# Kernel tuning notes

Hardware: AMD Instinct MI355X
Metric: run time of the kernel (lower is better)

Reference implementation:

```python
import jax, jax.numpy as jnp
import numpy as np

N, D, H, B, K = 65536, 64, 128, 16, 16
EPS = 0.0

def setup_inputs() -> dict:
    key = jax.random.key(0)
    ks = jax.random.split(key, 5)
    x = jax.random.normal(ks[0], (N, D), dtype=jnp.float32)
    pos = jax.random.normal(ks[1], (N, 3), dtype=jnp.float32)
    batch = (jnp.arange(N, dtype=jnp.int32) // (N // B)).astype(jnp.int32)
    W1 = jax.random.normal(ks[2], (D, H), dtype=jnp.float32) * (1.0 / np.sqrt(D))
    b1 = jnp.zeros((H,), dtype=jnp.float32)
    W2 = jax.random.normal(ks[3], (H, D), dtype=jnp.float32) * (1.0 / np.sqrt(H))
    b2 = jnp.zeros((D,), dtype=jnp.float32)
    return {"x": x, "pos": pos, "batch": batch, "W1": W1, "b1": b1, "W2": W2, "b2": b2}

def reference(x, pos, batch, W1, b1, W2, b2):
    # batch is assumed contiguous with B equal segments of n nodes each
    n = N // B
    pos_s = pos.reshape(B, n, 3)
    x_s = x.reshape(B, n, D)
    # pairwise squared distances per segment via gram trick: [B, n, n]
    sq = jnp.sum(pos_s * pos_s, axis=-1)
    d2 = sq[:, :, None] + sq[:, None, :] - 2.0 * jnp.einsum('bic,bjc->bij', pos_s, pos_s)
    # exclude self-loops (loop=False in knn_graph)
    d2 = jnp.where(jnp.eye(n, dtype=bool)[None], jnp.inf, d2)
    # k nearest neighbors per node: indices [B, n, K]
    _, idx = jax.lax.top_k(-d2, K)
    # GIN sum aggregation: gather neighbor features and sum over K
    nb = x_s[jnp.arange(B)[:, None, None], idx]        # [B, n, K, D]
    agg = nb.sum(axis=2).reshape(N, D)                  # [N, D]
    h = (1.0 + EPS) * x + agg
    h = jax.nn.relu(h @ W1 + b1)
    out = h @ W2 + b2
    return out
```

## Files before the change

kernel.cpp:

```cpp
#include <hip/hip_runtime.h>
#include <math.h>

#define DIM  64
#define HID  128
#define KNN  16
#define SEG  1024
#define TSZ  128
#define CAP  12

typedef unsigned long long u64;
#define INF_BITS 0x7F800000u

__device__ __forceinline__ void ins16(float (&bd)[KNN], int (&bi)[KNN],
                                      float d, int g) {
    float cd = d; int ci = g;
    #pragma unroll
    for (int i = 0; i < KNN; ++i) {
        bool lt = cd < bd[i];
        float dl = lt ? cd : bd[i];
        float dh = lt ? bd[i] : cd;
        int   il = lt ? ci : bi[i];
        int   ih = lt ? bi[i] : ci;
        bd[i] = dl; bi[i] = il; cd = dh; ci = ih;
    }
}

__device__ __forceinline__ void drain_buf(const u64* bufe, int tid,
        float (&bd)[KNN], int (&bi)[KNN], int& cnt,
        unsigned* thrU, int l) {
    for (int t = 0; t < CAP; ++t) {
        if (__ballot(t < cnt) == 0ull) break;
        u64 e = bufe[t * 256 + tid];
        float d = __uint_as_float((unsigned)e);
        int   g = (int)(e >> 32);
        if ((t < cnt) && (d < bd[KNN - 1])) ins16(bd, bi, d, g);
    }
    cnt = 0;
    atomicMin(&thrU[l], __float_as_uint(bd[KNN - 1]));
}

struct f2 { float a, b; };
__device__ __forceinline__ f2 f2mul(f2 x, float s) {
    #pragma clang fp contract(off)
    f2 r; r.a = x.a * s; r.b = x.b * s; return r;
}
__device__ __forceinline__ f2 f2add(f2 x, f2 y) {
    #pragma clang fp contract(off)
    f2 r; r.a = x.a + y.a; r.b = x.b + y.b; return r;
}
__device__ __forceinline__ f2 f2adds(f2 x, float s) {
    #pragma clang fp contract(off)
    f2 r; r.a = s + x.a; r.b = s + x.b; return r;
}
__device__ __forceinline__ f2 f2sub(f2 x, f2 y) {
    #pragma clang fp contract(off)
    f2 r; r.a = x.a - y.a; r.b = x.b - y.b; return r;
}

template<bool CHECK>
__device__ __forceinline__ void knn_scan(
    const float* __restrict__ pos, int bbase, int segbase, int qlocal, int l,
    float qx, float qy, float qz, float qs,
    float* tx, float* ty, float* tz, float* ts,
    u64* bufe, unsigned* thrU, volatile unsigned* thrv, int tid,
    float (&bd)[KNN], int (&bi)[KNN])
{
    #pragma clang fp contract(off)
    int cnt = 0;

    #pragma unroll
    for (int m = 0; m < 2; ++m) {
        int t = (m << 6) + l;
        int g = (bbase + segbase + t) * 3;
        float ax = pos[g], ay = pos[g + 1], az = pos[g + 2];
        tx[t] = ax; ty[t] = ay; tz[t] = az;
        ts[t] = (ax * ax + ay * ay) + az * az;
    }

    __syncthreads();

    #pragma unroll
    for (int k = 0; k < KNN; ++k) { bd[k] = INFINITY; bi[k] = 0x7FFFFFFF; }
    for (int jj = 0; jj < KNN; ++jj) {
        float ax = tx[jj], ay = ty[jj], az = tz[jj], as = ts[jj];
        float dot = (ax * qx + ay * qy) + az * qz;
        float d2  = (qs + as) - 2.0f * dot;
        int cj = segbase + jj;
        if (cj == qlocal) d2 = INFINITY;
        ins16(bd, bi, d2, cj);
    }
    atomicMin(&thrU[l], __float_as_uint(bd[KNN - 1]));

    int jstart = KNN;
    for (int tb = 0; tb < SEG; tb += TSZ) {
        if (tb > 0) {
            #pragma unroll
            for (int m = 0; m < 2; ++m) {
                int t = (m << 6) + l;
                int g = (bbase + segbase + tb + t) * 3;
                float ax = pos[g], ay = pos[g + 1], az = pos[g + 2];
                tx[t] = ax; ty[t] = ay; tz[t] = az;
                ts[t] = (ax * ax + ay * ay) + az * az;
            }
        }
        for (int j = jstart; j < TSZ; j += 4) {
            float tl = __uint_as_float(thrv[l]);
            float4 X = *(const float4*)(tx + j);
            float4 Y = *(const float4*)(ty + j);
            float4 Z = *(const float4*)(tz + j);
            float4 S = *(const float4*)(ts + j);
            const int c0 = segbase + tb + j;

            {   f2 Px = {X.x, X.y}, Py = {Y.x, Y.y}, Pz = {Z.x, Z.y}, Ps = {S.x, S.y};
                f2 dot = f2add(f2add(f2mul(Px, qx), f2mul(Py, qy)), f2mul(Pz, qz));
                f2 d2  = f2sub(f2adds(Ps, qs), f2mul(dot, 2.0f));
                if (CHECK) {
                    if (c0     == qlocal) d2.a = INFINITY;
                    if (c0 + 1 == qlocal) d2.b = INFINITY;
                }
                if (d2.a <= tl) {
                    bufe[cnt * 256 + tid] =
                        ((u64)(unsigned)c0 << 32) | __float_as_uint(d2.a); ++cnt; }
                if (d2.b <= tl) {
                    bufe[cnt * 256 + tid] =
                        ((u64)(unsigned)(c0 + 1) << 32) | __float_as_uint(d2.b); ++cnt; }
            }
            {   f2 Px = {X.z, X.w}, Py = {Y.z, Y.w}, Pz = {Z.z, Z.w}, Ps = {S.z, S.w};
                f2 dot = f2add(f2add(f2mul(Px, qx), f2mul(Py, qy)), f2mul(Pz, qz));
                f2 d2  = f2sub(f2adds(Ps, qs), f2mul(dot, 2.0f));
                if (CHECK) {
                    if (c0 + 2 == qlocal) d2.a = INFINITY;
                    if (c0 + 3 == qlocal) d2.b = INFINITY;
                }
                if (d2.a <= tl) {
                    bufe[cnt * 256 + tid] =
                        ((u64)(unsigned)(c0 + 2) << 32) | __float_as_uint(d2.a); ++cnt; }
                if (d2.b <= tl) {
                    bufe[cnt * 256 + tid] =
                        ((u64)(unsigned)(c0 + 3) << 32) | __float_as_uint(d2.b); ++cnt; }
            }

            if (__ballot(cnt >= CAP - 4) != 0ull)
                drain_buf(bufe, tid, bd, bi, cnt, thrU, l);
        }
        jstart = 0;
    }
    drain_buf(bufe, tid, bd, bi, cnt, thrU, l);
}

__global__ __launch_bounds__(256, 4) void knn_agg(
    const float* __restrict__ x, const float* __restrict__ pos,
    float* __restrict__ agg_out)
{
    __shared__ u64 smem[4160];

    const int tid = threadIdx.x;
    const int w   = tid >> 6;
    const int l   = tid & 63;

    const int qb     = blockIdx.x;
    const int batch  = qb >> 6;
    const int bbase  = batch << 12;
    const int qlocal = ((qb & 63) << 6) + l;
    const int qglob  = bbase + qlocal;

    float* tilef = (float*)smem;
    float* tx = tilef + w * 512;
    float* ty = tx + TSZ;
    float* tz = tx + 2 * TSZ;
    float* ts = tx + 3 * TSZ;
    unsigned* thrU = (unsigned*)(tilef + 2048);
    u64* bufe = smem + 1056;

    if (tid < 64) thrU[tid] = INF_BITS;

    float qx, qy, qz, qs;
    {
        #pragma clang fp contract(off)
        qx = pos[3 * qglob + 0];
        qy = pos[3 * qglob + 1];
        qz = pos[3 * qglob + 2];
        qs = (qx * qx + qy * qy) + qz * qz;
    }

    float bd[KNN]; int bi[KNN];
    const int segbase = w << 10;
    const int wself   = (qb & 63) >> 4;
    if (w == wself)
        knn_scan<true >(pos, bbase, segbase, qlocal, l, qx, qy, qz, qs,
                        tx, ty, tz, ts, bufe, thrU, thrU, tid, bd, bi);
    else
        knn_scan<false>(pos, bbase, segbase, qlocal, l, qx, qy, qz, qs,
                        tx, ty, tz, ts, bufe, thrU, thrU, tid, bd, bi);

    __syncthreads();

    float* md  = (float*)smem;
    int*  midx = (int*)(smem + 2048);
    #pragma unroll
    for (int k = 0; k < KNN; ++k) {
        int slot = (w << 4) + k;
        md[slot * 64 + l]   = bd[k];
        midx[slot * 64 + l] = bi[k];
    }
    __syncthreads();

    if (tid < 64) {
        float bd2[KNN]; int bi2[KNN];
        #pragma unroll
        for (int k = 0; k < KNN; ++k) {
            bd2[k] = md[k * 64 + tid];
            bi2[k] = midx[k * 64 + tid];
        }
        for (int c = KNN; c < 64; ++c) {
            float d = md[c * 64 + tid];
            int   g = midx[c * 64 + tid];
            if (d < bd2[KNN - 1]) ins16(bd2, bi2, d, g);
        }
        int* mi2 = (int*)smem;
        #pragma unroll
        for (int k = 0; k < KNN; ++k) mi2[k * 64 + tid] = bi2[k];
    }
    __syncthreads();

    {
        const int* mi2 = (const int*)smem;
        const int r  = tid >> 2;
        const int p  = tid & 3;
        const int q  = (qb << 6) + r;
        const int cb = p << 4;

        int idxs[KNN];
        #pragma unroll
        for (int k = 0; k < KNN; ++k) idxs[k] = mi2[k * 64 + r];

        float4 a0 = *(const float4*)(x + (size_t)q * DIM + cb + 0);
        float4 a1 = *(const float4*)(x + (size_t)q * DIM + cb + 4);
        float4 a2 = *(const float4*)(x + (size_t)q * DIM + cb + 8);
        float4 a3 = *(const float4*)(x + (size_t)q * DIM + cb + 12);

        #pragma unroll 4
        for (int k = 0; k < KNN; ++k) {
            const float* nr = x + (size_t)(bbase + idxs[k]) * DIM + cb;
            float4 v0 = *(const float4*)(nr + 0);
            float4 v1 = *(const float4*)(nr + 4);
            float4 v2 = *(const float4*)(nr + 8);
            float4 v3 = *(const float4*)(nr + 12);
            a0.x += v0.x; a0.y += v0.y; a0.z += v0.z; a0.w += v0.w;
            a1.x += v1.x; a1.y += v1.y; a1.z += v1.z; a1.w += v1.w;
            a2.x += v2.x; a2.y += v2.y; a2.z += v2.z; a2.w += v2.w;
            a3.x += v3.x; a3.y += v3.y; a3.z += v3.z; a3.w += v3.w;
        }

        float* o = agg_out + (size_t)q * DIM + cb;
        *(float4*)(o + 0)  = a0;
        *(float4*)(o + 4)  = a1;
        *(float4*)(o + 8)  = a2;
        *(float4*)(o + 12) = a3;
    }
}

__global__ void prep(const float* __restrict__ W1, float* __restrict__ w1t) {
    int e = blockIdx.x * 256 + threadIdx.x;
    int k = e >> 7, j = e & 127;
    w1t[j * 64 + k] = W1[e];
}

__global__ __launch_bounds__(256, 1) void mlp(
    const float* __restrict__ w1t, const float* __restrict__ b1,
    const float* __restrict__ W2, const float* __restrict__ b2,
    float* __restrict__ io)
{
    const int row = blockIdx.x * 256 + threadIdx.x;

    float xv[DIM];
    {
        const float4* xr = (const float4*)(io + (size_t)row * DIM);
        #pragma unroll
        for (int i = 0; i < 16; ++i) {
            float4 v = xr[i];
            xv[4*i] = v.x; xv[4*i+1] = v.y; xv[4*i+2] = v.z; xv[4*i+3] = v.w;
        }
    }

    float acc[DIM];
    #pragma unroll
    for (int c = 0; c < DIM; ++c) acc[c] = b2[c];

    for (int j = 0; j < HID; ++j) {
        const float* w1 = w1t + j * DIM;
        float s0 = 0.f, s1 = 0.f, s2 = 0.f, s3 = 0.f;
        #pragma unroll
        for (int c = 0; c < DIM; c += 4) {
            s0 = fmaf(w1[c + 0], xv[c + 0], s0);
            s1 = fmaf(w1[c + 1], xv[c + 1], s1);
            s2 = fmaf(w1[c + 2], xv[c + 2], s2);
            s3 = fmaf(w1[c + 3], xv[c + 3], s3);
        }
        float h = fmaxf((s0 + s1) + (s2 + s3) + b1[j], 0.0f);

        const float* w2 = W2 + j * DIM;
        #pragma unroll
        for (int c = 0; c < DIM; ++c)
            acc[c] = fmaf(h, w2[c], acc[c]);
    }

    float4* o = (float4*)(io + (size_t)row * DIM);
    #pragma unroll
    for (int i = 0; i < 16; ++i)
        o[i] = make_float4(acc[4*i], acc[4*i+1], acc[4*i+2], acc[4*i+3]);
}

extern "C" void kernel_launch(void* const* d_in, const int* in_sizes, int n_in,
                              void* d_out, int out_size, void* d_ws, size_t ws_size,
                              hipStream_t stream) {
    (void)in_sizes; (void)n_in; (void)ws_size; (void)out_size;
    const float* x   = (const float*)d_in[0];
    const float* pos = (const float*)d_in[1];
    const float* W1  = (const float*)d_in[3];
    const float* b1  = (const float*)d_in[4];
    const float* W2  = (const float*)d_in[5];
    const float* b2  = (const float*)d_in[6];
    float* out = (float*)d_out;
    float* w1t = (float*)d_ws;

    prep<<<dim3(32), dim3(256), 0, stream>>>(W1, w1t);
    knn_agg<<<dim3(1024), dim3(256), 0, stream>>>(x, pos, out);
    mlp<<<dim3(256), dim3(256), 0, stream>>>(w1t, b1, W2, b2, out);
}
```

Before: 417.3 us.

## Unroll KNN scan by 8 with warp-level early reject; split MLP hidden dim across threads

The KNN scan now handles 8 candidates per iteration and skips all buffer-insertion work when no lane in the wavefront has a candidate below its threshold. Separately, the MLP kernel splits the 128 hidden units across two thread halves per row, doubling the grid to 512 blocks. The halves' partial outputs are combined through LDS. The MLP change targets the low occupancy of the single-block-per-CU, 256-block launch. The costs are more register pressure in the scan, an extra LDS round trip and a barrier in the MLP, and the shared buffer shrinking slightly.

```diff
diff --git a/kernel.cpp b/kernel.cpp
--- a/kernel.cpp
+++ b/kernel.cpp
@@ -55,6 +55,11 @@
 __device__ __forceinline__ f2 f2sub(f2 x, f2 y) {
     #pragma clang fp contract(off)
     f2 r; r.a = x.a - y.a; r.b = x.b - y.b; return r;
+}
+__device__ __forceinline__ f2 d2pair(f2 Px, f2 Py, f2 Pz, f2 Ps,
+                                     float qx, float qy, float qz, float qs) {
+    f2 dot = f2add(f2add(f2mul(Px, qx), f2mul(Py, qy)), f2mul(Pz, qz));
+    return f2sub(f2adds(Ps, qs), f2mul(dot, 2.0f));
 }
 
 template<bool CHECK>
@@ -103,45 +108,70 @@
                 ts[t] = (ax * ax + ay * ay) + az * az;
             }
         }
-        for (int j = jstart; j < TSZ; j += 4) {
+        for (int j = jstart; j < TSZ; j += 8) {
             float tl = __uint_as_float(thrv[l]);
-            float4 X = *(const float4*)(tx + j);
-            float4 Y = *(const float4*)(ty + j);
-            float4 Z = *(const float4*)(tz + j);
-            float4 S = *(const float4*)(ts + j);
+            float4 X0 = *(const float4*)(tx + j);
+            float4 X1 = *(const float4*)(tx + j + 4);
+            float4 Y0 = *(const float4*)(ty + j);
+            float4 Y1 = *(const float4*)(ty + j + 4);
+            float4 Z0 = *(const float4*)(tz + j);
+            float4 Z1 = *(const float4*)(tz + j + 4);
+            float4 S0 = *(const float4*)(ts + j);
+            float4 S1 = *(const float4*)(ts + j + 4);
             const int c0 = segbase + tb + j;
 
-            {   f2 Px = {X.x, X.y}, Py = {Y.x, Y.y}, Pz = {Z.x, Z.y}, Ps = {S.x, S.y};
-                f2 dot = f2add(f2add(f2mul(Px, qx), f2mul(Py, qy)), f2mul(Pz, qz));
-                f2 d2  = f2sub(f2adds(Ps, qs), f2mul(dot, 2.0f));
-                if (CHECK) {
-                    if (c0     == qlocal) d2.a = INFINITY;
-                    if (c0 + 1 == qlocal) d2.b = INFINITY;
-                }
-                if (d2.a <= tl) {
-                    bufe[cnt * 256 + tid] =
-                        ((u64)(unsigned)c0 << 32) | __float_as_uint(d2.a); ++cnt; }
-                if (d2.b <= tl) {
-                    bufe[cnt * 256 + tid] =
-                        ((u64)(unsigned)(c0 + 1) << 32) | __float_as_uint(d2.b); ++cnt; }
+            f2 dA = d2pair({X0.x, X0.y}, {Y0.x, Y0.y}, {Z0.x, Z0.y}, {S0.x, S0.y},
+                           qx, qy, qz, qs);
+            f2 dB = d2pair({X0.z, X0.w}, {Y0.z, Y0.w}, {Z0.z, Z0.w}, {S0.z, S0.w},
+                           qx, qy, qz, qs);
+            f2 dC = d2pair({X1.x, X1.y}, {Y1.x, Y1.y}, {Z1.x, Z1.y}, {S1.x, S1.y},
+                           qx, qy, qz, qs);
+            f2 dD = d2pair({X1.z, X1.w}, {Y1.z, Y1.w}, {Z1.z, Z1.w}, {S1.z, S1.w},
+                           qx, qy, qz, qs);
+            if (CHECK) {
+                int s = qlocal - c0;
+                if (s == 0) dA.a = INFINITY;
+                if (s == 1) dA.b = INFINITY;
+                if (s == 2) dB.a = INFINITY;
+                if (s == 3) dB.b = INFINITY;
+                if (s == 4) dC.a = INFINITY;
+                if (s == 5) dC.b = INFINITY;
+                if (s == 6) dD.a = INFINITY;
+                if (s == 7) dD.b = INFINITY;
             }
-            {   f2 Px = {X.z, X.w}, Py = {Y.z, Y.w}, Pz = {Z.z, Z.w}, Ps = {S.z, S.w};
-                f2 dot = f2add(f2add(f2mul(Px, qx), f2mul(Py, qy)), f2mul(Pz, qz));
-                f2 d2  = f2sub(f2adds(Ps, qs), f2mul(dot, 2.0f));
-                if (CHECK) {
-                    if (c0 + 2 == qlocal) d2.a = INFINITY;
-                    if (c0 + 3 == qlocal) d2.b = INFINITY;
-                }
-                if (d2.a <= tl) {
-                    bufe[cnt * 256 + tid] =
-                        ((u64)(unsigned)(c0 + 2) << 32) | __float_as_uint(d2.a); ++cnt; }
-                if (d2.b <= tl) {
-                    bufe[cnt * 256 + tid] =
-                        ((u64)(unsigned)(c0 + 3) << 32) | __float_as_uint(d2.b); ++cnt; }
+            float mn = fminf(fminf(fminf(dA.a, dA.b), fminf(dB.a, dB.b)),
+                             fminf(fminf(dC.a, dC.b), fminf(dD.a, dD.b)));
+
+            if (__ballot(mn <= tl) != 0ull) {
+                if (dA.a <= tl) {
+                    bufe[cnt * 256 + tid] =
+                        ((u64)(unsigned)(c0 + 0) << 32) | __float_as_uint(dA.a); ++cnt; }
+                if (dA.b <= tl) {
+                    bufe[cnt * 256 + tid] =
+                        ((u64)(unsigned)(c0 + 1) << 32) | __float_as_uint(dA.b); ++cnt; }
+                if (dB.a <= tl) {
+                    bufe[cnt * 256 + tid] =
+                        ((u64)(unsigned)(c0 + 2) << 32) | __float_as_uint(dB.a); ++cnt; }
+                if (dB.b <= tl) {
+                    bufe[cnt * 256 + tid] =
+                        ((u64)(unsigned)(c0 + 3) << 32) | __float_as_uint(dB.b); ++cnt; }
+                if (__ballot(cnt >= CAP - 4) != 0ull)
+                    drain_buf(bufe, tid, bd, bi, cnt, thrU, l);
+                if (dC.a <= tl) {
+                    bufe[cnt * 256 + tid] =
+                        ((u64)(unsigned)(c0 + 4) << 32) | __float_as_uint(dC.a); ++cnt; }
+                if (dC.b <= tl) {
+                    bufe[cnt * 256 + tid] =
+                        ((u64)(unsigned)(c0 + 5) << 32) | __float_as_uint(dC.b); ++cnt; }
+                if (dD.a <= tl) {
+                    bufe[cnt * 256 + tid] =
+                        ((u64)(unsigned)(c0 + 6) << 32) | __float_as_uint(dD.a); ++cnt; }
+                if (dD.b <= tl) {
+                    bufe[cnt * 256 + tid] =
+                        ((u64)(unsigned)(c0 + 7) << 32) | __float_as_uint(dD.b); ++cnt; }
+                if (__ballot(cnt >= CAP - 4) != 0ull)
+                    drain_buf(bufe, tid, bd, bi, cnt, thrU, l);
             }
-
-            if (__ballot(cnt >= CAP - 4) != 0ull)
-                drain_buf(bufe, tid, bd, bi, cnt, thrU, l);
         }
         jstart = 0;
     }
@@ -152,7 +182,7 @@
     const float* __restrict__ x, const float* __restrict__ pos,
     float* __restrict__ agg_out)
 {
-    __shared__ u64 smem[4160];
+    __shared__ u64 smem[4128];
 
     const int tid = threadIdx.x;
     const int w   = tid >> 6;
@@ -266,12 +296,17 @@
     w1t[j * 64 + k] = W1[e];
 }
 
-__global__ __launch_bounds__(256, 1) void mlp(
+__global__ __launch_bounds__(256, 2) void mlp(
     const float* __restrict__ w1t, const float* __restrict__ b1,
     const float* __restrict__ W2, const float* __restrict__ b2,
     float* __restrict__ io)
 {
-    const int row = blockIdx.x * 256 + threadIdx.x;
+    __shared__ float hl[128 * 65];
+
+    const int tid  = threadIdx.x;
+    const int r    = tid & 127;
+    const int half = tid >> 7;
+    const int row  = blockIdx.x * 128 + r;
 
     float xv[DIM];
     {
@@ -285,9 +320,12 @@
 
     float acc[DIM];
     #pragma unroll
-    for (int c = 0; c < DIM; ++c) acc[c] = b2[c];
-
-    for (int j = 0; j < HID; ++j) {
+    for (int c = 0; c < DIM; ++c) acc[c] = 0.0f;
+
+    const int jb = half << 6;
+    #pragma unroll 2
+    for (int jj = 0; jj < 64; ++jj) {
+        const int j = jb + jj;
         const float* w1 = w1t + j * DIM;
         float s0 = 0.f, s1 = 0.f, s2 = 0.f, s3 = 0.f;
         #pragma unroll
@@ -305,10 +343,23 @@
             acc[c] = fmaf(h, w2[c], acc[c]);
     }
 
-    float4* o = (float4*)(io + (size_t)row * DIM);
-    #pragma unroll
-    for (int i = 0; i < 16; ++i)
-        o[i] = make_float4(acc[4*i], acc[4*i+1], acc[4*i+2], acc[4*i+3]);
+    if (half == 0) {
+        #pragma unroll
+        for (int c = 0; c < DIM; ++c) hl[r * 65 + c] = acc[c];
+    }
+    __syncthreads();
+    if (half == 1) {
+        float* o = io + (size_t)row * DIM;
+        #pragma unroll
+        for (int c = 0; c < DIM; c += 4) {
+            float4 r4;
+            r4.x = acc[c + 0] + hl[r * 65 + c + 0] + b2[c + 0];
+            r4.y = acc[c + 1] + hl[r * 65 + c + 1] + b2[c + 1];
+            r4.z = acc[c + 2] + hl[r * 65 + c + 2] + b2[c + 2];
+            r4.w = acc[c + 3] + hl[r * 65 + c + 3] + b2[c + 3];
+            *(float4*)(o + c) = r4;
+        }
+    }
 }
 
 extern "C" void kernel_launch(void* const* d_in, const int* in_sizes, int n_in,
@@ -326,5 +377,5 @@
 
     prep<<<dim3(32), dim3(256), 0, stream>>>(W1, w1t);
     knn_agg<<<dim3(1024), dim3(256), 0, stream>>>(x, pos, out);
-    mlp<<<dim3(256), dim3(256), 0, stream>>>(w1t, b1, W2, b2, out);
-}
+    mlp<<<dim3(512), dim3(256), 0, stream>>>(w1t, b1, W2, b2, out);
+}
```

After: 459.4 us. 10.1% more time.
